# Optimization experiments

Measured on AMD Instinct MI355X. Metric: run time of the kernel, lower is better.

## Reference

```python
import jax, jax.numpy as jnp
import numpy as np

B, T, C = 8, 2048, 1024
H, D = 16, 64
DLOW = 64  # D_DECAY = D_AAA = D_MV = D_GATE = 64
EPS_LN = 1e-5


def setup_inputs() -> dict:
    key = jax.random.key(0)
    ks = jax.random.split(key, 26)
    p = lambda k, shape, s=0.02: (jax.random.normal(k, shape, jnp.float32) * s)
    u = lambda k, shape: jax.random.uniform(k, shape, jnp.float32)
    return {
        "x":   jax.random.normal(ks[0], (B, T, C), jnp.float32),
        # token-shift mix coefficients (1,1,C)
        "x_r": u(ks[1], (1, 1, C)), "x_w": u(ks[2], (1, 1, C)),
        "x_k": u(ks[3], (1, 1, C)), "x_v": u(ks[4], (1, 1, C)),
        "x_a": u(ks[5], (1, 1, C)), "x_g": u(ks[6], (1, 1, C)),
        # decay lora: w1 [C,DLOW], w2 [DLOW,H], w0 [1,1,H,1]
        "w0": p(ks[7], (1, 1, H, 1)), "w1": p(ks[8], (C, DLOW)), "w2": p(ks[9], (DLOW, H)),
        # in-context lr lora
        "a0": p(ks[10], (1, 1, H, 1)), "a1": p(ks[11], (C, DLOW)), "a2": p(ks[12], (DLOW, H)),
        # value residual lora
        "v0": p(ks[13], (1, 1, C)), "v1": p(ks[14], (C, DLOW)), "v2": p(ks[15], (DLOW, C)),
        # gate lora
        "g1": p(ks[16], (C, DLOW)), "g2": p(ks[17], (DLOW, C)),
        "k_k": 0.85 + p(ks[18], (1, 1, C)),
        "r_k": p(ks[19], (H, D)),
        # main projections, stored [in, out] so x @ W matches nn.Linear
        "Wr": p(ks[20], (C, C)), "Wk": p(ks[21], (C, C)),
        "Wv": p(ks[22], (C, C)), "Wo": p(ks[23], (C, C)),
        # GroupNorm(n_head, n_embd) affine params
        "ln_w": jnp.ones((C,), jnp.float32) + p(ks[24], (C,)),
        "ln_b": p(ks[25], (C,)),
    }


def reference(x, x_r, x_w, x_k, x_v, x_a, x_g,
              w0, w1, w2, a0, a1, a2, v0, v1, v2, g1, g2,
              k_k, r_k, Wr, Wk, Wv, Wo, ln_w, ln_b):
    Bb, Tt, Cc = x.shape
    Hh, Dd = r_k.shape
    # token shift: sx = x_t - x_{t-1} (zero-padded)
    xx = jnp.concatenate([jnp.zeros((Bb, 1, Cc), x.dtype), x[:, :-1]], axis=1)
    sx = x - xx
    xr = x + sx * x_r
    xw = x + sx * x_w
    xk = x + sx * x_k
    xv = x + sx * x_v
    xa = x + sx * x_a
    xg = x + sx * x_g

    r = (xr @ Wr).reshape(Bb, Tt, Hh, Dd)
    # decay in (0, exp(-0.5)): exp(-softplus(-(w0 + lora)) - 0.5)
    w = jnp.exp(-jax.nn.softplus(-(w0 + (jnp.tanh(xw @ w1) @ w2).reshape(Bb, Tt, Hh, 1))) - 0.5)
    k = xk @ Wk
    v = xv @ Wv
    v_res_gate = jax.nn.sigmoid(v0 + jnp.tanh(xv @ v1) @ v2)
    v = v + (v - v) * v_res_gate  # no-op, kept for faithfulness
    a = jax.nn.sigmoid(a0 + (jnp.tanh(xa @ a1) @ a2).reshape(Bb, Tt, Hh, 1))
    g = jax.nn.sigmoid(jnp.tanh(xg @ g1) @ g2)

    kk = (k * k_k).reshape(Bb, Tt, Hh, Dd)
    kk = kk / jnp.maximum(jnp.linalg.norm(kk, axis=-1, keepdims=True), 1e-12)
    vh = v.reshape(Bb, Tt, Hh, Dd)

    # WKV linear recurrence: state = state * w_t + kk_t * v_t * a_t
    kv = (kk * vh * a).astype(jnp.float32)            # [B,T,H,D]
    w_t = jnp.moveaxis(w.astype(jnp.float32), 1, 0)   # [T,B,H,1]
    kv_t = jnp.moveaxis(kv, 1, 0)                     # [T,B,H,D]

    def step(state, inputs):
        wt, kvt = inputs
        state = state * wt + kvt
        return state, state

    init = jnp.zeros((Bb, Hh, Dd), jnp.float32)
    _, states = jax.lax.scan(step, init, (w_t, kv_t))  # [T,B,H,D]
    x_wkv = jnp.moveaxis(states, 0, 1).astype(x.dtype)  # [B,T,H,D]

    x_wkv = x_wkv * r
    bonus = jnp.sum(r * kk * r_k, axis=-1, keepdims=True) * vh
    x_wkv = x_wkv + bonus  # [B,T,H,D]

    # GroupNorm(H groups over C channels), per (B*T) sample
    mean = x_wkv.mean(axis=-1, keepdims=True)
    var = x_wkv.var(axis=-1, keepdims=True)
    xn = (x_wkv - mean) * jax.lax.rsqrt(var + EPS_LN)
    xn = xn.reshape(Bb, Tt, Cc) * ln_w + ln_b

    return (xn * g) @ Wo
```

## Files before the change

### kernel.cpp

```cpp
#include <hip/hip_runtime.h>


typedef __bf16 bf16;
typedef __attribute__((ext_vector_type(8))) __bf16 bf16x8;
typedef __attribute__((ext_vector_type(4))) float f32x4;

#define TBTOK 16384
#define TSEQ  2048
#define CDIM  1024
#define HN    16
#define CHUNK 32
#define NCH   64

__device__ __forceinline__ float wredsum(float v) {
#pragma unroll
  for (int o = 32; o > 0; o >>= 1) v += __shfl_xor(v, o, 64);
  return v;
}
__device__ __forceinline__ float redsum8(float v) {
#pragma unroll
  for (int o = 4; o > 0; o >>= 1) v += __shfl_xor(v, o, 64);
  return v;
}
__device__ __forceinline__ float sigmf(float x) { return 1.f / (1.f + expf(-x)); }

__device__ __forceinline__ void gl_lds16(const bf16* g, bf16* l) {
  __builtin_amdgcn_global_load_lds(
      (const __attribute__((address_space(1))) unsigned int*)g,
      (__attribute__((address_space(3))) unsigned int*)l, 16, 0, 0);
}

__global__ __launch_bounds__(256) void prep_kern(
    const float* __restrict__ x, const float* __restrict__ mr,
    const float* __restrict__ mk, const float* __restrict__ mv,
    bf16* __restrict__ xr, bf16* __restrict__ xk, bf16* __restrict__ xv,
    bf16* __restrict__ xbf,
    const float* __restrict__ Wr, const float* __restrict__ Wk,
    const float* __restrict__ Wv, const float* __restrict__ Wo,
    const float* __restrict__ w1, const float* __restrict__ a1, const float* __restrict__ g1,
    const float* __restrict__ mw, const float* __restrict__ ma, const float* __restrict__ mg,
    const float* __restrict__ g2, const float* __restrict__ w2, const float* __restrict__ a2,
    bf16* __restrict__ WrT, bf16* __restrict__ WkT, bf16* __restrict__ WvT, bf16* __restrict__ WoT,
    bf16* __restrict__ Bcat, bf16* __restrict__ g2T,
    bf16* __restrict__ w2T, bf16* __restrict__ a2T, float* __restrict__ zpad) {
  int bid0 = blockIdx.x;
  int tid = threadIdx.x;
  if (bid0 < 8192) {
    long i8 = ((long)bid0 * 256 + tid) * 8;
    int m = (int)(i8 >> 10);
    int c = (int)(i8 & 1023);
    f32x4 x0 = *(const f32x4*)(x + i8);
    f32x4 x1 = *(const f32x4*)(x + i8 + 4);
    f32x4 p0 = {0.f, 0.f, 0.f, 0.f}, p1 = {0.f, 0.f, 0.f, 0.f};
    if ((m & (TSEQ - 1)) != 0) {
      p0 = *(const f32x4*)(x + i8 - CDIM);
      p1 = *(const f32x4*)(x + i8 - CDIM + 4);
    }
    f32x4 r0 = *(const f32x4*)(mr + c), r1 = *(const f32x4*)(mr + c + 4);
    f32x4 k0 = *(const f32x4*)(mk + c), k1 = *(const f32x4*)(mk + c + 4);
    f32x4 v0 = *(const f32x4*)(mv + c), v1 = *(const f32x4*)(mv + c + 4);
    bf16x8 or_, ok_, ov_, ox_;
#pragma unroll
    for (int j = 0; j < 4; j++) {
      float s0 = x0[j] - p0[j], s1 = x1[j] - p1[j];
      or_[j] = (bf16)(x0[j] + s0 * r0[j]); or_[4 + j] = (bf16)(x1[j] + s1 * r1[j]);
      ok_[j] = (bf16)(x0[j] + s0 * k0[j]); ok_[4 + j] = (bf16)(x1[j] + s1 * k1[j]);
      ov_[j] = (bf16)(x0[j] + s0 * v0[j]); ov_[4 + j] = (bf16)(x1[j] + s1 * v1[j]);
      ox_[j] = (bf16)x0[j];                ox_[4 + j] = (bf16)x1[j];
    }
    *(bf16x8*)(xr + i8) = or_;
    *(bf16x8*)(xk + i8) = ok_;
    *(bf16x8*)(xv + i8) = ov_;
    *(bf16x8*)(xbf + i8) = ox_;
    return;
  }
  int bid = bid0 - 8192;
  int tx = tid & 31, ty = tid >> 5;
  __shared__ bf16 tile[32][33];
  if (bid < 4096) {
    int sel = bid >> 10, t = bid & 1023;
    int k0 = (t >> 5) * 32, n0 = (t & 31) * 32;
    const float* src = sel == 0 ? Wr : (sel == 1 ? Wk : (sel == 2 ? Wv : Wo));
    bf16* dst = sel == 0 ? WrT : (sel == 1 ? WkT : (sel == 2 ? WvT : WoT));
#pragma unroll
    for (int i = 0; i < 4; i++)
      tile[ty + i * 8][tx] = (bf16)src[(long)(k0 + ty + i * 8) * 1024 + n0 + tx];
    __syncthreads();
#pragma unroll
    for (int i = 0; i < 4; i++)
      dst[(long)(n0 + ty + i * 8) * 1024 + k0 + tx] = tile[tx][ty + i * 8];
  } else if (bid < 4480) {
    int idx = bid - 4096;
    int mat = idx >> 7, rem = idx & 127;
    int half = rem >> 6, t = rem & 63;
    int k0 = (t >> 1) * 32, n0 = (t & 1) * 32;
    const float* W = mat == 0 ? w1 : (mat == 1 ? a1 : g1);
    const float* mx = mat == 0 ? mw : (mat == 1 ? ma : mg);
#pragma unroll
    for (int i = 0; i < 4; i++) {
      int k = k0 + ty + i * 8;
      float s = half == 0 ? (1.f + mx[k]) : (-mx[k]);
      tile[ty + i * 8][tx] = (bf16)(s * W[(long)k * 64 + n0 + tx]);
    }
    __syncthreads();
#pragma unroll
    for (int i = 0; i < 4; i++)
      Bcat[(long)(mat * 64 + n0 + ty + i * 8) * 2048 + half * 1024 + k0 + tx] =
          tile[tx][ty + i * 8];
  } else if (bid < 4544) {
    int t = bid - 4480;
    int k0 = (t >> 5) * 32, n0 = (t & 31) * 32;
#pragma unroll
    for (int i = 0; i < 4; i++)
      tile[ty + i * 8][tx] = (bf16)g2[(long)(k0 + ty + i * 8) * 1024 + n0 + tx];
    __syncthreads();
#pragma unroll
    for (int i = 0; i < 4; i++)
      g2T[(long)(n0 + ty + i * 8) * 64 + k0 + tx] = tile[tx][ty + i * 8];
  } else {
#pragma unroll
    for (int rep = 0; rep < 4; rep++) {
      int idx = rep * 256 + tid;
      int k = idx >> 4, h = idx & 15;
      w2T[h * 64 + k] = (bf16)w2[idx];
      a2T[h * 64 + k] = (bf16)a2[idx];
    }
    if (tid < 64) zpad[tid] = 0.f;
  }
}

#define BARRIER __builtin_amdgcn_s_barrier()
#define LGKM0                                              \
  do {                                                     \
    asm volatile("s_waitcnt lgkmcnt(0)" ::: "memory");     \
    __builtin_amdgcn_sched_barrier(0);                     \
  } while (0)

#define READ_A(HALFP, QM)                                                                \
  {                                                                                      \
    const bf16* _h = (HALFP);                                                            \
    _Pragma("unroll") for (int i = 0; i < 4; i++) {                                      \
      int ra = (QM)*64 + i * 16 + lr;                                                    \
      _Pragma("unroll") for (int ks = 0; ks < 2; ks++)                                   \
          af[i][ks] = *(const bf16x8*)&_h[ra * 64 + (((ks * 4 + quad) ^ (ra & 7)) * 8)]; \
    }                                                                                    \
  }

#define READ_B(HALFP, QN)                                                                \
  {                                                                                      \
    const bf16* _h = (HALFP);                                                            \
    _Pragma("unroll") for (int jj = 0; jj < 2; jj++) {                                   \
      int rb = bro + ((QN)*2 + jj) * 16 + lr;                                            \
      _Pragma("unroll") for (int ks = 0; ks < 2; ks++)                                   \
          bfr[(QN)*2 + jj][ks] =                                                         \
              *(const bf16x8*)&_h[rb * 64 + (((ks * 4 + quad) ^ (rb & 7)) * 8)];         \
    }                                                                                    \
  }

#define MFMA16(QM, QN)                                                            \
  __builtin_amdgcn_s_setprio(1);                                                  \
  _Pragma("unroll") for (int ks = 0; ks < 2; ks++)                                \
  _Pragma("unroll") for (int i = 0; i < 4; i++)                                   \
  _Pragma("unroll") for (int jj = 0; jj < 2; jj++)                                \
      acc[(QM)*4 + i][(QN)*2 + jj] = __builtin_amdgcn_mfma_f32_16x16x32_bf16(     \
          af[i][ks], bfr[(QN)*2 + jj][ks], acc[(QM)*4 + i][(QN)*2 + jj], 0, 0, 0);\
  __builtin_amdgcn_s_setprio(0);

template <typename OT>
__global__ __launch_bounds__(512, 2) void gemm256_kern(
    const bf16* __restrict__ A0, const bf16* __restrict__ A1, const bf16* __restrict__ A2,
    const bf16* __restrict__ BT0, const bf16* __restrict__ BT1, const bf16* __restrict__ BT2,
    OT* __restrict__ out0, OT* __restrict__ out1, OT* __restrict__ out2,
    int K, int nbpm) {
  int nwg = gridDim.x;
  int id = blockIdx.x;
  int qq = nwg >> 3;
  int wg = (id & 7) * qq + (id >> 3);
  int mat = wg / nbpm;
  int rem = wg - mat * nbpm;
  int m0 = (rem & 63) << 8;
  int n0 = (rem >> 6) << 8;
  const bf16* Am = mat == 0 ? A0 : (mat == 1 ? A1 : A2);
  const bf16* BTm = mat == 0 ? BT0 : (mat == 1 ? BT1 : BT2);
  OT* out = mat == 0 ? out0 : (mat == 1 ? out1 : out2);

  __shared__ bf16 Al[2][2][128 * 64];
  __shared__ bf16 Bl[2][2][128 * 64];

  int tid = threadIdx.x;
  int w = tid >> 6, lane = tid & 63, quad = lane >> 4, lr = lane & 15;
  int wr = w >> 2, wc = w & 3;
  int hb = wc >> 1, bro = (wc & 1) * 64;

  int swz = ((tid & 7) ^ ((tid >> 3) & 7)) * 8;
  const bf16* aBase = Am + (long)(m0 + (tid >> 3)) * K + swz;
  const bf16* bBase = BTm + (long)(n0 + (tid >> 3)) * K + swz;

  auto stgA = [&](int db, int h, int t) {
    const bf16* g = aBase + (long)(h * 128) * K + t * 64;
    bf16* l = &Al[db][h][0] + w * 512;
    gl_lds16(g, l);
    gl_lds16(g + (long)64 * K, l + 4096);
  };
  auto stgB = [&](int db, int h, int t) {
    const bf16* g = bBase + (long)(h * 128) * K + t * 64;
    bf16* l = &Bl[db][h][0] + w * 512;
    gl_lds16(g, l);
    gl_lds16(g + (long)64 * K, l + 4096);
  };

  const bf16* A0p = &Al[0][wr][0];
  const bf16* A1p = &Al[1][wr][0];
  const bf16* B0p = &Bl[0][hb][0];
  const bf16* B1p = &Bl[1][hb][0];

  f32x4 acc[8][4] = {};
  bf16x8 af[4][2], bfr[4][2];

  int NT = K >> 6, NU = NT >> 1;

  stgB(0, 0, 0); stgB(0, 1, 0); stgA(0, 0, 0); stgA(0, 1, 0);
  stgB(1, 0, 1); stgB(1, 1, 1); stgA(1, 0, 1); stgA(1, 1, 1);
  asm volatile("s_waitcnt vmcnt(8)" ::: "memory");
  BARRIER;

#pragma unroll 1
  for (int u = 0; u < NU; u++) {
    int t2 = 2 * u + 2, t3 = 2 * u + 3;
    READ_A(A0p, 0);
    READ_B(B0p, 0);
    asm volatile("s_waitcnt lgkmcnt(8)" ::: "memory");
    BARRIER; LGKM0;
    MFMA16(0, 0);
    BARRIER;
    READ_B(B0p, 1);
    BARRIER; LGKM0;
    MFMA16(0, 1);
    BARRIER;
    READ_A(A0p, 1);
    if (t2 < NT) { stgB(0, 0, t2); stgB(0, 1, t2); }
    BARRIER; LGKM0;
    MFMA16(1, 1);
    BARRIER;
    if (t2 < NT) { stgA(0, 0, t2); stgA(0, 1, t2); }
    BARRIER;
    __builtin_amdgcn_sched_barrier(0);
    MFMA16(1, 0);
    if (t2 < NT) { asm volatile("s_waitcnt vmcnt(8)" ::: "memory"); }
    else         { asm volatile("s_waitcnt vmcnt(0)" ::: "memory"); }
    BARRIER;
    READ_A(A1p, 0);
    READ_B(B1p, 0);
    asm volatile("s_waitcnt lgkmcnt(8)" ::: "memory");
    BARRIER; LGKM0;
    MFMA16(0, 0);
    BARRIER;
    READ_B(B1p, 1);
    BARRIER; LGKM0;
    MFMA16(0, 1);
    BARRIER;
    READ_A(A1p, 1);
    if (t3 < NT) { stgB(1, 0, t3); stgB(1, 1, t3); }
    BARRIER; LGKM0;
    MFMA16(1, 1);
    BARRIER;
    if (t3 < NT) { stgA(1, 0, t3); stgA(1, 1, t3); }
    BARRIER;
    __builtin_amdgcn_sched_barrier(0);
    MFMA16(1, 0);
    if (t3 < NT) { asm volatile("s_waitcnt vmcnt(8)" ::: "memory"); }
    else         { asm volatile("s_waitcnt vmcnt(0)" ::: "memory"); }
    BARRIER;
  }

#pragma unroll
  for (int i = 0; i < 8; i++)
#pragma unroll
    for (int j = 0; j < 4; j++)
#pragma unroll
      for (int rg = 0; rg < 4; rg++) {
        int row = m0 + wr * 128 + i * 16 + quad * 4 + rg;
        int col = n0 + wc * 64 + j * 16 + lr;
        out[(long)row * CDIM + col] = (OT)acc[i][j][rg];
      }
}

__global__ __launch_bounds__(256) void stage1_kern(
    const bf16* __restrict__ xbf, const bf16* __restrict__ Bcat,
    const float* __restrict__ zpad, const bf16* __restrict__ w2T, const bf16* __restrict__ a2T,
    const float* __restrict__ w0, const float* __restrict__ a0,
    bf16* __restrict__ t1g, float* __restrict__ w_arr, float* __restrict__ a_arr) {
  int m0 = blockIdx.x * 64;
  __shared__ bf16 Abuf[3][64 * 64];
  __shared__ bf16 Bbuf[3][192 * 64];
  __shared__ bf16 Lt1[64 * 136];

  int tid = threadIdx.x;
  int w = tid >> 6, lane = tid & 63, quad = lane >> 4, lr = lane & 15;

  int r0 = tid >> 3, s0 = tid & 7;
  int c0 = (s0 ^ (r0 & 7)) * 8;
  const bf16* arow0 = xbf + (long)(m0 + r0) * CDIM + c0;
  const bf16* arow1 = xbf + (long)(m0 + 32 + r0) * CDIM + c0;
  bool fr0 = ((m0 + r0) & (TSEQ - 1)) == 0;
  const bf16* aprev0 = fr0 ? ((const bf16*)zpad) : (arow0 - CDIM);
  const bf16* aprev1 = arow1 - CDIM;
  long pm0 = fr0 ? 0 : 64;
  const bf16* brow = Bcat + (long)r0 * 2048 + c0;

  bf16* sA0 = &Abuf[0][0]; bf16* sA1 = &Abuf[1][0]; bf16* sA2 = &Abuf[2][0];
  bf16* sB0 = &Bbuf[0][0]; bf16* sB1 = &Bbuf[1][0]; bf16* sB2 = &Bbuf[2][0];

  auto stage = [&](bf16* sA, bf16* sB, int kk) {
    const bf16* a0s = (kk < 16) ? (arow0 + kk * 64) : (aprev0 + (long)(kk - 16) * pm0);
    const bf16* a1s = (kk < 16) ? (arow1 + kk * 64) : (aprev1 + (long)(kk - 16) * 64);
    gl_lds16(a0s, sA + w * 512);
    gl_lds16(a1s, sA + 2048 + w * 512);
    const bf16* bs = brow + kk * 64;
#pragma unroll
    for (int j = 0; j < 6; j++)
      gl_lds16(bs + (long)j * 32 * 2048, sB + j * 2048 + w * 512);
  };

  f32x4 acc[4][3] = {};

  stage(sA0, sB0, 0);
  stage(sA1, sB1, 1);
  stage(sA2, sB2, 2);
  asm volatile("s_waitcnt vmcnt(16)" ::: "memory");
  BARRIER;

#pragma unroll 1
  for (int t = 0; t < 32; t++) {
    bf16x8 af[4][2], bfr[3][2];
#pragma unroll
    for (int i = 0; i < 4; i++) {
      int ra = i * 16 + lr;
#pragma unroll
      for (int ks = 0; ks < 2; ks++)
        af[i][ks] = *(const bf16x8*)&sA0[ra * 64 + (((ks * 4 + quad) ^ (ra & 7)) * 8)];
    }
#pragma unroll
    for (int n = 0; n < 3; n++) {
      int rb = w * 48 + n * 16 + lr;
#pragma unroll
      for (int ks = 0; ks < 2; ks++)
        bfr[n][ks] = *(const bf16x8*)&sB0[rb * 64 + (((ks * 4 + quad) ^ (rb & 7)) * 8)];
    }
    LGKM0;
    __builtin_amdgcn_s_setprio(1);
#pragma unroll
    for (int ks = 0; ks < 2; ks++)
#pragma unroll
      for (int i = 0; i < 4; i++)
#pragma unroll
        for (int n = 0; n < 3; n++)
          acc[i][n] = __builtin_amdgcn_mfma_f32_16x16x32_bf16(af[i][ks], bfr[n][ks],
                                                              acc[i][n], 0, 0, 0);
    __builtin_amdgcn_s_setprio(0);
    BARRIER;
    if (t + 3 < 32) {
      stage(sA0, sB0, t + 3);
      asm volatile("s_waitcnt vmcnt(16)" ::: "memory");
    } else if (t == 29) {
      asm volatile("s_waitcnt vmcnt(8)" ::: "memory");
    } else if (t == 30) {
      asm volatile("s_waitcnt vmcnt(0)" ::: "memory");
    }
    BARRIER;
    bf16* tmpA = sA0; sA0 = sA1; sA1 = sA2; sA2 = tmpA;
    bf16* tmpB = sB0; sB0 = sB1; sB1 = sB2; sB2 = tmpB;
  }

#pragma unroll
  for (int i = 0; i < 4; i++)
#pragma unroll
    for (int n = 0; n < 3; n++) {
      int col = w * 48 + n * 16 + lr;
#pragma unroll
      for (int rg = 0; rg < 4; rg++) {
        int row = i * 16 + quad * 4 + rg;
        float tv = tanhf(acc[i][n][rg]);
        if (col < 128) Lt1[row * 136 + col] = (bf16)tv;
        else t1g[(long)(m0 + row) * 64 + (col - 128)] = (bf16)tv;
      }
    }
  __syncthreads();
#pragma unroll
  for (int rep = 0; rep < 4; rep++) {
    int idx = rep * 256 + tid;
    int row = idx >> 4, h = idx & 15;
    const bf16* rw = &Lt1[row * 136];
    const bf16* ra = rw + 64;
    const bf16* ww = w2T + h * 64;
    const bf16* aw = a2T + h * 64;
    float dw = 0.f, da = 0.f;
#pragma unroll
    for (int k = 0; k < 64; k++) {
      dw += (float)rw[k] * (float)ww[k];
      da += (float)ra[k] * (float)aw[k];
    }
    w_arr[h * TBTOK + m0 + row] = 0.60653066f * sigmf(w0[h] + dw);
    a_arr[h * TBTOK + m0 + row] = sigmf(a0[h] + da);
  }
}

__global__ __launch_bounds__(256) void scan1_kern(
    const bf16* __restrict__ k_buf, const bf16* __restrict__ v_buf, const bf16* __restrict__ r_buf,
    const float* __restrict__ k_k, const float* __restrict__ r_k,
    const float* __restrict__ a_arr, const float* __restrict__ w_arr,
    float* __restrict__ kv2, float* __restrict__ Parr, float* __restrict__ bonus,
    float* __restrict__ Lend) {
  int wid = blockIdx.x * 4 + (threadIdx.x >> 6);
  int lane = threadIdx.x & 63;
  int bh = wid >> 6, c = wid & 63;
  int b = bh >> 4, h = bh & 15;
  int mstart = b * TSEQ + c * CHUNK;
  int kc = h * 64 + lane;
  float kkc = k_k[kc], rkc = r_k[kc];
  float st = 0.f, cw = 1.f;
  long mbase = (long)mstart * CDIM + kc;
  int hm = h * TBTOK + mstart;
  long sbase = ((long)hm) * 64 + lane;
  float kf = (float)k_buf[mbase] * kkc;
  float vf = (float)v_buf[mbase];
  float rf = (float)r_buf[mbase];
  float af = a_arr[hm];
  float wt = w_arr[hm];
  for (int t = 0; t < CHUNK; t++) {
    float kf_n = 0.f, vf_n = 0.f, rf_n = 0.f, af_n = 0.f, wt_n = 0.f;
    if (t < CHUNK - 1) {
      kf_n = (float)k_buf[mbase + CDIM] * kkc;
      vf_n = (float)v_buf[mbase + CDIM];
      rf_n = (float)r_buf[mbase + CDIM];
      af_n = a_arr[hm + 1];
      wt_n = w_arr[hm + 1];
    }
    float ss = wredsum(kf * kf);
    float kkn = kf / fmaxf(sqrtf(ss), 1e-12f);
    st = st * wt + kkn * vf * af;
    kv2[sbase] = st;
    cw *= wt;
    float bs = wredsum(rf * kkn * rkc);
    if (lane == 0) {
      Parr[hm] = cw;
      bonus[(mstart + t) * HN + h] = bs;
    }
    kf = kf_n; vf = vf_n; rf = rf_n; af = af_n; wt = wt_n;
    mbase += CDIM; hm += 1; sbase += 64;
  }
  Lend[(long)wid * 64 + lane] = st;
}

__global__ __launch_bounds__(256) void gate_post_kern(
    const bf16* __restrict__ t1g, const bf16* __restrict__ g2T,
    const float* __restrict__ kv2, const float* __restrict__ Parr,
    const float* __restrict__ Lend, const float* __restrict__ bonus,
    bf16* __restrict__ r_buf, const bf16* __restrict__ v_buf,
    const float* __restrict__ ln_w, const float* __restrict__ ln_b) {
  int ncol0 = blockIdx.x * 128;
  int m0 = blockIdx.y * 128;

  __shared__ bf16 Al[128 * 32];
  __shared__ bf16 Bl[128 * 32];
  __shared__ bf16 gtile[128 * 136];

  int tid = threadIdx.x;
  int w = tid >> 6, lane = tid & 63, quad = lane >> 4, lr = lane & 15;
  int wm = (w & 1) * 64, wn = (w >> 1) * 64;

  f32x4 acc[4][4] = {};

  int r0 = tid >> 2, kc0 = (tid & 3) * 8;
  const bf16* ag0 = t1g + (long)(m0 + r0) * 64 + kc0;
  const bf16* ag1 = ag0 + (long)64 * 64;
  const bf16* bg0 = g2T + (long)(ncol0 + r0) * 64 + kc0;
  const bf16* bg1 = bg0 + (long)64 * 64;
  bf16* la0 = Al + w * 512;
  bf16* la1 = Al + 2048 + w * 512;
  bf16* lb0 = Bl + w * 512;
  bf16* lb1 = Bl + 2048 + w * 512;

  for (int k0 = 0; k0 < 64; k0 += 32) {
    gl_lds16(ag0, la0);
    gl_lds16(ag1, la1);
    gl_lds16(bg0, lb0);
    gl_lds16(bg1, lb1);
    ag0 += 32; ag1 += 32; bg0 += 32; bg1 += 32;
    __syncthreads();
    bf16x8 af[4], bff[4];
#pragma unroll
    for (int i = 0; i < 4; i++) af[i] = *(const bf16x8*)&Al[(wm + i * 16 + lr) * 32 + quad * 8];
#pragma unroll
    for (int j = 0; j < 4; j++) bff[j] = *(const bf16x8*)&Bl[(wn + j * 16 + lr) * 32 + quad * 8];
#pragma unroll
    for (int i = 0; i < 4; i++)
#pragma unroll
      for (int j = 0; j < 4; j++)
        acc[i][j] = __builtin_amdgcn_mfma_f32_16x16x32_bf16(af[i], bff[j], acc[i][j], 0, 0, 0);
    __syncthreads();
  }
#pragma unroll
  for (int i = 0; i < 4; i++)
#pragma unroll
    for (int j = 0; j < 4; j++)
#pragma unroll
      for (int rg = 0; rg < 4; rg++) {
        int row = wm + i * 16 + quad * 4 + rg;
        int col = wn + j * 16 + lr;
        gtile[row * 136 + col] = (bf16)sigmf(acc[i][j][rg]);
      }
  __syncthreads();

  int c_loc = (tid & 15) * 8;
  int col_g = ncol0 + c_loc;
  int h = col_g >> 6;
  int d0 = col_g & 63;
  f32x4 lnw0 = *(const f32x4*)(ln_w + col_g);
  f32x4 lnw1 = *(const f32x4*)(ln_w + col_g + 4);
  f32x4 lnb0 = *(const f32x4*)(ln_b + col_g);
  f32x4 lnb1 = *(const f32x4*)(ln_b + col_g + 4);
#pragma unroll
  for (int jj = 0; jj < 8; jj++) {
    int row = jj * 16 + (tid >> 4);
    int row_g = m0 + row;
    int b = row_g >> 11;
    int ch = (row_g & (TSEQ - 1)) >> 5;
    long kvb = ((long)h * TBTOK + row_g) * 64 + d0;
    f32x4 st0 = *(const f32x4*)(kv2 + kvb);
    f32x4 st1 = *(const f32x4*)(kv2 + kvb + 4);
    f32x4 cy0 = {0.f, 0.f, 0.f, 0.f}, cy1 = {0.f, 0.f, 0.f, 0.f};
    if (ch != 0) {
      long lb = ((long)((b * 16 + h) * NCH + ch - 1)) * 64 + d0;
      cy0 = *(const f32x4*)(Lend + lb);
      cy1 = *(const f32x4*)(Lend + lb + 4);
    }
    float pw = Parr[h * TBTOK + row_g];
    float bs = bonus[row_g * HN + h];
    long rb = (long)row_g * CDIM + col_g;
    bf16x8 rf8 = *(const bf16x8*)(r_buf + rb);
    bf16x8 vf8 = *(const bf16x8*)(v_buf + rb);
    bf16x8 g8 = *(const bf16x8*)&gtile[row * 136 + c_loc];
    float xw[8];
#pragma unroll
    for (int q = 0; q < 4; q++) {
      xw[q]     = (st0[q] + pw * cy0[q]) * (float)rf8[q]     + bs * (float)vf8[q];
      xw[4 + q] = (st1[q] + pw * cy1[q]) * (float)rf8[4 + q] + bs * (float)vf8[4 + q];
    }
    float sum = 0.f;
#pragma unroll
    for (int q = 0; q < 8; q++) sum += xw[q];
    float mn = redsum8(sum) * (1.f / 64.f);
    float vs = 0.f;
#pragma unroll
    for (int q = 0; q < 8; q++) {
      xw[q] -= mn;
      vs += xw[q] * xw[q];
    }
    float var = redsum8(vs) * (1.f / 64.f);
    float rq = rsqrtf(var + 1e-5f);
    bf16x8 o8;
#pragma unroll
    for (int q = 0; q < 4; q++) {
      o8[q]     = (bf16)((xw[q] * rq * lnw0[q] + lnb0[q]) * (float)g8[q]);
      o8[4 + q] = (bf16)((xw[4 + q] * rq * lnw1[q] + lnb1[q]) * (float)g8[4 + q]);
    }
    *(bf16x8*)(r_buf + rb) = o8;
  }
}

extern "C" void kernel_launch(void* const* d_in, const int* in_sizes, int n_in,
                              void* d_out, int out_size, void* d_ws, size_t ws_size,
                              hipStream_t stream) {
  const float* x    = (const float*)d_in[0];
  const float* x_r  = (const float*)d_in[1];
  const float* x_w  = (const float*)d_in[2];
  const float* x_k  = (const float*)d_in[3];
  const float* x_v  = (const float*)d_in[4];
  const float* x_a  = (const float*)d_in[5];
  const float* x_g  = (const float*)d_in[6];
  const float* w0   = (const float*)d_in[7];
  const float* w1   = (const float*)d_in[8];
  const float* w2   = (const float*)d_in[9];
  const float* a0   = (const float*)d_in[10];
  const float* a1   = (const float*)d_in[11];
  const float* a2   = (const float*)d_in[12];
  const float* g1   = (const float*)d_in[16];
  const float* g2   = (const float*)d_in[17];
  const float* k_k  = (const float*)d_in[18];
  const float* r_k  = (const float*)d_in[19];
  const float* Wr   = (const float*)d_in[20];
  const float* Wk   = (const float*)d_in[21];
  const float* Wv   = (const float*)d_in[22];
  const float* Wo   = (const float*)d_in[23];
  const float* ln_w = (const float*)d_in[24];
  const float* ln_b = (const float*)d_in[25];
  float* out = (float*)d_out;

  char* p = (char*)d_ws;
  auto carve = [&](size_t bytes) {
    void* r = (void*)p;
    p += (bytes + 255) & ~(size_t)255;
    return r;
  };
  bf16* WrT = (bf16*)carve(1024 * 1024 * 2);
  bf16* WkT = (bf16*)carve(1024 * 1024 * 2);
  bf16* WvT = (bf16*)carve(1024 * 1024 * 2);
  bf16* WoT = (bf16*)carve(1024 * 1024 * 2);
  bf16* Bcat = (bf16*)carve(192 * 2048 * 2);
  bf16* g2T  = (bf16*)carve(1024 * 64 * 2);
  bf16* w2T  = (bf16*)carve(16 * 64 * 2);
  bf16* a2T  = (bf16*)carve(16 * 64 * 2);
  float* zpad = (float*)carve(64 * 4);
  bf16* t1g   = (bf16*)carve((size_t)TBTOK * 64 * 2);
  bf16* r_buf = (bf16*)carve((size_t)TBTOK * CDIM * 2);
  bf16* k_buf = (bf16*)carve((size_t)TBTOK * CDIM * 2);
  bf16* v_buf = (bf16*)carve((size_t)TBTOK * CDIM * 2);
  float* w_arr = (float*)carve((size_t)TBTOK * HN * 4);
  float* a_arr = (float*)carve((size_t)TBTOK * HN * 4);
  float* bonus = (float*)carve((size_t)TBTOK * HN * 4);
  float* Parr  = (float*)carve((size_t)TBTOK * HN * 4);
  float* Lend  = (float*)carve((size_t)128 * NCH * 64 * 4);
  bf16* xr  = (bf16*)carve((size_t)TBTOK * CDIM * 2);
  bf16* xk  = (bf16*)carve((size_t)TBTOK * CDIM * 2);
  bf16* xv  = (bf16*)carve((size_t)TBTOK * CDIM * 2);
  bf16* xbf = (bf16*)carve((size_t)TBTOK * CDIM * 2);
  float* kv2 = (float*)xv;

  prep_kern<<<dim3(8192 + 4545), 256, 0, stream>>>(
      x, x_r, x_k, x_v, xr, xk, xv, xbf,
      Wr, Wk, Wv, Wo, w1, a1, g1, x_w, x_a, x_g, g2, w2, a2,
      WrT, WkT, WvT, WoT, Bcat, g2T, w2T, a2T, zpad);
  stage1_kern<<<dim3(TBTOK / 64), 256, 0, stream>>>(
      xbf, Bcat, zpad, w2T, a2T, w0, a0, t1g, w_arr, a_arr);
  gemm256_kern<bf16><<<dim3(768), 512, 0, stream>>>(
      xr, xk, xv, WrT, WkT, WvT, r_buf, k_buf, v_buf, 1024, 256);
  scan1_kern<<<dim3(128 * NCH / 4), 256, 0, stream>>>(
      k_buf, v_buf, r_buf, k_k, r_k, a_arr, w_arr, kv2, Parr, bonus, Lend);
  gate_post_kern<<<dim3(8, TBTOK / 128), 256, 0, stream>>>(
      t1g, g2T, kv2, Parr, Lend, bonus, r_buf, v_buf, ln_w, ln_b);
  gemm256_kern<float><<<dim3(256), 512, 0, stream>>>(
      r_buf, r_buf, r_buf, WoT, WoT, WoT, out, out, out, 1024, 256);
}
```

Before: 517.7 us.

## Chain R/K/V GEMMs within each workgroup instead of separate tiles per matrix

The fused R/K/V projection GEMM previously launched 768 workgroups, one per output tile per matrix. Now 256 workgroups each compute the same output tile for all three matrices in sequence, continuing the double-buffered K-loop across matrix boundaries and flushing the accumulator to the right output at each boundary. The aim is to avoid a partial second wave and per-block prologue and epilogue costs on the GPU, and to keep the pipeline full across matrices. The cost is fewer, longer blocks, which lowers parallelism, and the mid-loop stores may stall the pipelined loads. Tile mapping also changes from M-major to N-fastest ordering, and addressing switches to 32-bit offsets.

Result: slower. 533.7 us (+3.1%).

```diff
diff --git a/kernel.cpp b/kernel.cpp
--- a/kernel.cpp
+++ b/kernel.cpp
@@ -166,23 +166,17 @@
           af[i][ks], bfr[(QN)*2 + jj][ks], acc[(QM)*4 + i][(QN)*2 + jj], 0, 0, 0);\
   __builtin_amdgcn_s_setprio(0);
 
-template <typename OT>
+template <typename OT, int NMATS>
 __global__ __launch_bounds__(512, 2) void gemm256_kern(
     const bf16* __restrict__ A0, const bf16* __restrict__ A1, const bf16* __restrict__ A2,
     const bf16* __restrict__ BT0, const bf16* __restrict__ BT1, const bf16* __restrict__ BT2,
-    OT* __restrict__ out0, OT* __restrict__ out1, OT* __restrict__ out2,
-    int K, int nbpm) {
+    OT* __restrict__ out0, OT* __restrict__ out1, OT* __restrict__ out2, int K) {
   int nwg = gridDim.x;
   int id = blockIdx.x;
   int qq = nwg >> 3;
   int wg = (id & 7) * qq + (id >> 3);
-  int mat = wg / nbpm;
-  int rem = wg - mat * nbpm;
-  int m0 = (rem & 63) << 8;
-  int n0 = (rem >> 6) << 8;
-  const bf16* Am = mat == 0 ? A0 : (mat == 1 ? A1 : A2);
-  const bf16* BTm = mat == 0 ? BT0 : (mat == 1 ? BT1 : BT2);
-  OT* out = mat == 0 ? out0 : (mat == 1 ? out1 : out2);
+  int m0 = (wg >> 2) << 8;
+  int n0 = (wg & 3) << 8;
 
   __shared__ bf16 Al[2][2][128 * 64];
   __shared__ bf16 Bl[2][2][128 * 64];
@@ -193,17 +187,21 @@
   int hb = wc >> 1, bro = (wc & 1) * 64;
 
   int swz = ((tid & 7) ^ ((tid >> 3) & 7)) * 8;
-  const bf16* aBase = Am + (long)(m0 + (tid >> 3)) * K + swz;
-  const bf16* bBase = BTm + (long)(n0 + (tid >> 3)) * K + swz;
+  unsigned aoff = (unsigned)(m0 + (tid >> 3)) * K + swz;
+  unsigned boff = (unsigned)(n0 + (tid >> 3)) * K + swz;
 
   auto stgA = [&](int db, int h, int t) {
-    const bf16* g = aBase + (long)(h * 128) * K + t * 64;
+    const bf16* Am = A0;
+    if (NMATS == 3) { int mt = t >> 4; Am = mt == 0 ? A0 : (mt == 1 ? A1 : A2); }
+    const bf16* g = Am + aoff + (long)(h * 128) * K + (t & 15) * 64;
     bf16* l = &Al[db][h][0] + w * 512;
     gl_lds16(g, l);
     gl_lds16(g + (long)64 * K, l + 4096);
   };
   auto stgB = [&](int db, int h, int t) {
-    const bf16* g = bBase + (long)(h * 128) * K + t * 64;
+    const bf16* Bm = BT0;
+    if (NMATS == 3) { int mt = t >> 4; Bm = mt == 0 ? BT0 : (mt == 1 ? BT1 : BT2); }
+    const bf16* g = Bm + boff + (long)(h * 128) * K + (t & 15) * 64;
     bf16* l = &Bl[db][h][0] + w * 512;
     gl_lds16(g, l);
     gl_lds16(g + (long)64 * K, l + 4096);
@@ -217,7 +215,21 @@
   f32x4 acc[8][4] = {};
   bf16x8 af[4][2], bfr[4][2];
 
-  int NT = K >> 6, NU = NT >> 1;
+  auto writeC = [&](OT* out) {
+#pragma unroll
+    for (int i = 0; i < 8; i++)
+#pragma unroll
+      for (int j = 0; j < 4; j++)
+#pragma unroll
+        for (int rg = 0; rg < 4; rg++) {
+          int row = m0 + wr * 128 + i * 16 + quad * 4 + rg;
+          int col = n0 + wc * 64 + j * 16 + lr;
+          out[(long)row * CDIM + col] = (OT)acc[i][j][rg];
+        }
+  };
+
+  int NTt = NMATS * (K >> 6);
+  int NU = NTt >> 1;
 
   stgB(0, 0, 0); stgB(0, 1, 0); stgA(0, 0, 0); stgA(0, 1, 0);
   stgB(1, 0, 1); stgB(1, 1, 1); stgA(1, 0, 1); stgA(1, 1, 1);
@@ -227,6 +239,14 @@
 #pragma unroll 1
   for (int u = 0; u < NU; u++) {
     int t2 = 2 * u + 2, t3 = 2 * u + 3;
+    if (NMATS == 3 && u != 0 && (u & 7) == 0) {
+      OT* o = (u >> 3) == 1 ? out0 : out1;
+      writeC(o);
+#pragma unroll
+      for (int i = 0; i < 8; i++)
+#pragma unroll
+        for (int j = 0; j < 4; j++) acc[i][j] = f32x4{0.f, 0.f, 0.f, 0.f};
+    }
     READ_A(A0p, 0);
     READ_B(B0p, 0);
     asm volatile("s_waitcnt lgkmcnt(8)" ::: "memory");
@@ -238,16 +258,16 @@
     MFMA16(0, 1);
     BARRIER;
     READ_A(A0p, 1);
-    if (t2 < NT) { stgB(0, 0, t2); stgB(0, 1, t2); }
+    if (t2 < NTt) { stgB(0, 0, t2); stgB(0, 1, t2); }
     BARRIER; LGKM0;
     MFMA16(1, 1);
     BARRIER;
-    if (t2 < NT) { stgA(0, 0, t2); stgA(0, 1, t2); }
+    if (t2 < NTt) { stgA(0, 0, t2); stgA(0, 1, t2); }
     BARRIER;
     __builtin_amdgcn_sched_barrier(0);
     MFMA16(1, 0);
-    if (t2 < NT) { asm volatile("s_waitcnt vmcnt(8)" ::: "memory"); }
-    else         { asm volatile("s_waitcnt vmcnt(0)" ::: "memory"); }
+    if (t2 < NTt) { asm volatile("s_waitcnt vmcnt(8)" ::: "memory"); }
+    else          { asm volatile("s_waitcnt vmcnt(0)" ::: "memory"); }
     BARRIER;
     READ_A(A1p, 0);
     READ_B(B1p, 0);
@@ -260,29 +280,20 @@
     MFMA16(0, 1);
     BARRIER;
     READ_A(A1p, 1);
-    if (t3 < NT) { stgB(1, 0, t3); stgB(1, 1, t3); }
+    if (t3 < NTt) { stgB(1, 0, t3); stgB(1, 1, t3); }
     BARRIER; LGKM0;
     MFMA16(1, 1);
     BARRIER;
-    if (t3 < NT) { stgA(1, 0, t3); stgA(1, 1, t3); }
+    if (t3 < NTt) { stgA(1, 0, t3); stgA(1, 1, t3); }
     BARRIER;
     __builtin_amdgcn_sched_barrier(0);
     MFMA16(1, 0);
-    if (t3 < NT) { asm volatile("s_waitcnt vmcnt(8)" ::: "memory"); }
-    else         { asm volatile("s_waitcnt vmcnt(0)" ::: "memory"); }
-    BARRIER;
-  }
-
-#pragma unroll
-  for (int i = 0; i < 8; i++)
-#pragma unroll
-    for (int j = 0; j < 4; j++)
-#pragma unroll
-      for (int rg = 0; rg < 4; rg++) {
-        int row = m0 + wr * 128 + i * 16 + quad * 4 + rg;
-        int col = n0 + wc * 64 + j * 16 + lr;
-        out[(long)row * CDIM + col] = (OT)acc[i][j][rg];
-      }
+    if (t3 < NTt) { asm volatile("s_waitcnt vmcnt(8)" ::: "memory"); }
+    else          { asm volatile("s_waitcnt vmcnt(0)" ::: "memory"); }
+    BARRIER;
+  }
+
+  writeC(NMATS == 3 ? out2 : out0);
 }
 
 __global__ __launch_bounds__(256) void stage1_kern(
@@ -633,12 +644,12 @@
       WrT, WkT, WvT, WoT, Bcat, g2T, w2T, a2T, zpad);
   stage1_kern<<<dim3(TBTOK / 64), 256, 0, stream>>>(
       xbf, Bcat, zpad, w2T, a2T, w0, a0, t1g, w_arr, a_arr);
-  gemm256_kern<bf16><<<dim3(768), 512, 0, stream>>>(
-      xr, xk, xv, WrT, WkT, WvT, r_buf, k_buf, v_buf, 1024, 256);
+  gemm256_kern<bf16, 3><<<dim3(256), 512, 0, stream>>>(
+      xr, xk, xv, WrT, WkT, WvT, r_buf, k_buf, v_buf, 1024);
   scan1_kern<<<dim3(128 * NCH / 4), 256, 0, stream>>>(
       k_buf, v_buf, r_buf, k_k, r_k, a_arr, w_arr, kv2, Parr, bonus, Lend);
   gate_post_kern<<<dim3(8, TBTOK / 128), 256, 0, stream>>>(
       t1g, g2T, kv2, Parr, Lend, bonus, r_buf, v_buf, ln_w, ln_b);
-  gemm256_kern<float><<<dim3(256), 512, 0, stream>>>(
-      r_buf, r_buf, r_buf, WoT, WoT, WoT, out, out, out, 1024, 256);
-}
+  gemm256_kern<float, 1><<<dim3(256), 512, 0, stream>>>(
+      r_buf, r_buf, r_buf, WoT, WoT, WoT, out, out, out, 1024);
+}
```
